# Kernel tuning notes

Measured on AMD Instinct MI355X. Metric: run time of the kernel, lower is better.

## Reference

```python
import jax, jax.numpy as jnp
import numpy as np

VOC, EMB, C, H, W, ANS = 10000, 300, 24, 8, 8, 1000
HID = 500          # lstm_hidden_size
GH = 100           # g_mlp hidden
B, L = 64, 32
O = H * W          # obj_num
CONCAT = 2 * C + HID  # 548


def setup_inputs() -> dict:
    key = jax.random.key(0)
    ks = jax.random.split(key, 20)
    inp = {}
    inp["sent_batch"] = jax.random.randint(ks[0], (B, L), 0, VOC)
    inp["conv_map_batch"] = jax.random.normal(ks[1], (B, C, H, W), jnp.float32)
    inp["sents_lengths"] = jax.random.randint(ks[2], (B,), 1, L + 1)
    # embedding table with padding_idx=0 zeroed
    emb = jax.random.normal(ks[3], (VOC, EMB), jnp.float32) * 0.02
    inp["embed_table"] = emb.at[0].set(0.0)
    # forward-direction LSTM params (torch gate order i,f,g,o)
    s_ih = 1.0 / np.sqrt(HID)
    inp["W_ih"] = jax.random.uniform(ks[4], (4 * HID, EMB), jnp.float32, -s_ih, s_ih)
    inp["W_hh"] = jax.random.uniform(ks[5], (4 * HID, HID), jnp.float32, -s_ih, s_ih)
    inp["b_ih"] = jax.random.uniform(ks[6], (4 * HID,), jnp.float32, -s_ih, s_ih)
    inp["b_hh"] = jax.random.uniform(ks[7], (4 * HID,), jnp.float32, -s_ih, s_ih)
    # random (non-learned) LSTM initial state, as torch.rand in init_hidden
    inp["h0"] = jax.random.uniform(ks[8], (B, HID), jnp.float32)
    inp["c0"] = jax.random.uniform(ks[9], (B, HID), jnp.float32)
    def lin(k, o, i):
        s = 1.0 / np.sqrt(i)
        kw, kb = jax.random.split(k)
        return (jax.random.uniform(kw, (o, i), jnp.float32, -s, s),
                jax.random.uniform(kb, (o,), jnp.float32, -s, s))
    inp["g1_w"], inp["g1_b"] = lin(ks[10], GH, CONCAT)
    inp["g2_w"], inp["g2_b"] = lin(ks[11], GH, GH)
    inp["f1_w"], inp["f1_b"] = lin(ks[12], GH, GH)
    inp["f2_w"], inp["f2_b"] = lin(ks[13], ANS, GH)
    return inp


def _lstm_final_h(emb, lengths, W_ih, W_hh, b_ih, b_hh, h0, c0):
    # emb: (B, L, EMB); returns final forward hidden at t = length-1 per example
    xs = jnp.swapaxes(emb, 0, 1)  # (L, B, EMB)
    ts = jnp.arange(emb.shape[1])
    bias = b_ih + b_hh
    def step(carry, inp):
        h, c = carry
        xt, t = inp
        gates = xt @ W_ih.T + h @ W_hh.T + bias
        i, f, g, o = jnp.split(gates, 4, axis=-1)
        i, f, o = jax.nn.sigmoid(i), jax.nn.sigmoid(f), jax.nn.sigmoid(o)
        g = jnp.tanh(g)
        c_new = f * c + i * g
        h_new = o * jnp.tanh(c_new)
        m = (t < lengths)[:, None]
        return (jnp.where(m, h_new, h), jnp.where(m, c_new, c)), None
    (h_T, _), _ = jax.lax.scan(step, (h0, c0), (xs, ts))
    return h_T  # (B, HID)


def reference(sent_batch, conv_map_batch, sents_lengths, embed_table,
              W_ih, W_hh, b_ih, b_hh, h0, c0,
              g1_w, g1_b, g2_w, g2_b, f1_w, f1_b, f2_w, f2_b):
    emb = embed_table[sent_batch]  # (B, L, EMB)
    q = _lstm_final_h(emb, sents_lengths, W_ih, W_hh, b_ih, b_hh, h0, c0)  # (B, HID)
    obj = jnp.transpose(conv_map_batch, (0, 2, 3, 1)).reshape(B, O, C)  # (B, O, C)
    # g_mlp layer 1, split to avoid materializing (B, O^2, 548):
    # pair (i,j): cat(q, obj_j, obj_i) -> partial sums broadcast-added
    q_part = q @ g1_w[:, :HID].T                    # (B, GH)
    j_part = obj @ g1_w[:, HID:HID + C].T           # (B, O, GH) -- conv_expand_1 block
    i_part = obj @ g1_w[:, HID + C:].T              # (B, O, GH) -- conv_expand_2 block
    h1 = jax.nn.relu(q_part[:, None, None, :] + i_part[:, :, None, :]
                     + j_part[:, None, :, :] + g1_b)  # (B, O, O, GH)
    h2 = jax.nn.relu(h1 @ g2_w.T + g2_b)              # (B, O, O, GH)
    g_sum = h2.sum(axis=(1, 2))                       # (B, GH)
    f = jax.nn.relu(g_sum @ f1_w.T + f1_b)
    f = jax.nn.relu(f @ f2_w.T + f2_b)                # (B, ANS)
    return jax.nn.log_softmax(f, axis=-1)
```

## Files before the change

kernel.cpp:

```cpp
#include <hip/hip_runtime.h>
#include <cmath>

#define BATCH 64
#define SEQL  32
#define EMBD  300
#define HIDD  500
#define NOBJ  64
#define GHID  100
#define ANSN  1000
#define MCOL  2048

#define GRP    4
#define GBATCH 16
#define BPG    25
#define UPB8   20
#define NBLK   (GRP*BPG)
#define SLOTP  32

#define KPADX  328
#define TCH    4

typedef _Float16 half8 __attribute__((ext_vector_type(8)));
typedef float    f32x4 __attribute__((ext_vector_type(4)));

__device__ __forceinline__ float sigmf(float x){ return 1.f/(1.f+expf(-x)); }

__device__ __forceinline__ unsigned long long ld_cc8(const unsigned long long* p){
    return __hip_atomic_load(p, __ATOMIC_RELAXED, __HIP_MEMORY_SCOPE_AGENT);
}
__device__ __forceinline__ void st_cc8(_Float16* p, unsigned long long v){
    __hip_atomic_store((unsigned long long*)p, v, __ATOMIC_RELAXED, __HIP_MEMORY_SCOPE_AGENT);
}

__global__ __launch_bounds__(256, 1) void k_xg2(
    const int* __restrict__ sent, const float* __restrict__ table,
    const float* __restrict__ Wih, const float* __restrict__ b_ih,
    const float* __restrict__ b_hh, float* __restrict__ xgT, int* __restrict__ slots)
{
    __shared__ _Float16 Sh[64*KPADX];
    __shared__ int sidx[TCH][64];
    int tid = threadIdx.x;
    int tc = blockIdx.x;
    int n0 = blockIdx.y * 64;
    int w = tid >> 6, lane = tid & 63;
    int rA = lane & 15, kb = lane >> 4;

    if (tc == 0 && blockIdx.y == 0 && tid < NBLK)
        __hip_atomic_store(slots + tid*SLOTP, 0, __ATOMIC_RELAXED, __HIP_MEMORY_SCOPE_AGENT);

    for (int i = tid; i < TCH*64; i += 256){
        int tt = i >> 6, b = i & 63;
        sidx[tt][b] = sent[b*SEQL + tc*TCH + tt];
    }
    for (int i = tid; i < 64*75; i += 256){
        int n = i / 75, c4 = i - (i/75)*75;
        float4 v = {0.f,0.f,0.f,0.f};
        if (n0 + n < 2000)
            v = *(const float4*)(Wih + (size_t)(n0+n)*300 + c4*4);
        _Float16* dst = &Sh[n*KPADX + c4*4];
        dst[0]=(_Float16)v.x; dst[1]=(_Float16)v.y; dst[2]=(_Float16)v.z; dst[3]=(_Float16)v.w;
    }
    for (int i = tid; i < 64*20; i += 256){
        int n = i / 20, k = 300 + (i - (i/20)*20);
        Sh[n*KPADX + k] = (_Float16)0.f;
    }
    __syncthreads();
    half8 areg[10];
    #pragma unroll
    for (int ks = 0; ks < 10; ++ks)
        areg[ks] = *(const half8*)&Sh[(w*16 + rA)*KPADX + ks*32 + kb*8];
    float biasr[4];
    #pragma unroll
    for (int r = 0; r < 4; ++r){
        int n = n0 + w*16 + kb*4 + r;
        biasr[r] = (n < 2000) ? b_ih[n] + b_hh[n] : 0.f;
    }
    __syncthreads();

    for (int tt = 0; tt < TCH; ++tt){
        for (int i = tid; i < 64*75; i += 256){
            int m = i / 75, c4 = i - (i/75)*75;
            float4 v = *(const float4*)(table + (size_t)sidx[tt][m]*300 + c4*4);
            _Float16* dst = &Sh[m*KPADX + c4*4];
            dst[0]=(_Float16)v.x; dst[1]=(_Float16)v.y; dst[2]=(_Float16)v.z; dst[3]=(_Float16)v.w;
        }
        for (int i = tid; i < 64*20; i += 256){
            int m = i / 20, k = 300 + (i - (i/20)*20);
            Sh[m*KPADX + k] = (_Float16)0.f;
        }
        __syncthreads();

        f32x4 acc[4] = {};
        #pragma unroll
        for (int ks = 0; ks < 10; ++ks){
            #pragma unroll
            for (int mc = 0; mc < 4; ++mc){
                half8 bf = *(const half8*)&Sh[(mc*16 + rA)*KPADX + ks*32 + kb*8];
                acc[mc] = __builtin_amdgcn_mfma_f32_16x16x32_f16(areg[ks], bf, acc[mc], 0, 0, 0);
            }
        }
        #pragma unroll
        for (int r = 0; r < 4; ++r){
            int n = n0 + w*16 + kb*4 + r;
            if (n < 2000){
                #pragma unroll
                for (int mc = 0; mc < 4; ++mc)
                    xgT[(size_t)n*MCOL + (tc*TCH+tt)*64 + mc*16 + rA] = acc[mc][r] + biasr[r];
            }
        }
        __syncthreads();
    }
}

__device__ __forceinline__ void gbarA(int* slots, int grp, int ub, int seq)
{
    __syncthreads();
    if (threadIdx.x == 0)
        __hip_atomic_store(slots + (grp*BPG + ub)*SLOTP, seq,
                           __ATOMIC_RELAXED, __HIP_MEMORY_SCOPE_AGENT);
    if (threadIdx.x < BPG){
        int* s = slots + (grp*BPG + threadIdx.x)*SLOTP;
        while (__hip_atomic_load(s, __ATOMIC_RELAXED, __HIP_MEMORY_SCOPE_AGENT) < seq)
            __builtin_amdgcn_s_sleep(1);
    }
    asm volatile("" ::: "memory");
    __syncthreads();
}

__global__ __launch_bounds__(320, 1) void k_lstm_v9(
    _Float16* __restrict__ hF, float* __restrict__ hqB,
    const float* __restrict__ xgT, const float* __restrict__ Whh,
    const float* __restrict__ h0, const float* __restrict__ c0,
    const int* __restrict__ lens, int* __restrict__ slots)
{
    __shared__ _Float16 Wl[80*512];
    __shared__ float    gl[4*80*16];
    __shared__ _Float16 hout[16*UPB8];

    int tid = threadIdx.x, bid = blockIdx.x;
    int grp = bid / BPG, ub = bid - grp*BPG;
    int u0  = ub * UPB8;
    int w   = tid >> 6, lane = tid & 63;

    int pb  = tid & 15, puu = tid >> 4;
    int pu  = u0 + puu;
    int gb  = grp*GBATCH + pb;
    float cprev = c0[gb*HIDD + pu];
    float hprev = h0[gb*HIDD + pu];
    int   mylen = lens[gb];
    hout[pb*UPB8 + puu] = (_Float16)hprev;

    for (int i = tid; i < 80*512; i += 320){
        int m = i >> 9, k = i & 511;
        int g = m / UPB8, uu = m - g*UPB8;
        float v = (k < HIDD) ? Whh[(size_t)(g*HIDD + u0 + uu)*HIDD + k] : 0.f;
        int off = (i*2) ^ ((m & 7) << 4);
        *(_Float16*)((char*)Wl + off) = (_Float16)v;
    }
    __syncthreads();
    if (tid < 80){
        int b = tid / 5, q = tid - (tid/5)*5;
        unsigned long long v = *(const unsigned long long*)((const char*)hout + b*40 + q*8);
        st_cc8(hF + ((size_t)(1*GRP + grp)*GBATCH + b)*512 + u0 + q*4, v);
    }
    if (ub == 0 && tid >= 128 && tid < 224){
        int j = tid - 128;
        int buf = j / 48, r = j - buf*48;
        int b = r / 3, q = r - (r/3)*3;
        st_cc8(hF + ((size_t)(buf*GRP + grp)*GBATCH + b)*512 + 500 + q*4, 0ULL);
    }
    gbarA(slots, grp, ub, 1);

    const int mA = lane & 15, kb = lane >> 4;

    for (int t = 0; t < SEQL; ++t){
        const _Float16* hsrc = hF + (size_t)(((t&1)^1)*GRP + grp)*GBATCH*512;

        float xgv[4];
        #pragma unroll
        for (int g = 0; g < 4; ++g)
            xgv[g] = xgT[(size_t)(g*HIDD + pu)*MCOL + t*64 + gb];

        if (w < 4){
            half8 bf[4];
            #pragma unroll
            for (int ks4 = 0; ks4 < 4; ++ks4){
                int ke = (w*4 + ks4)*32 + kb*8;
                const unsigned long long* p =
                    (const unsigned long long*)(hsrc + mA*512 + ke);
                union { unsigned long long q[2]; half8 h; } u;
                u.q[0] = ld_cc8(p);
                u.q[1] = ld_cc8(p + 1);
                bf[ks4] = u.h;
            }
            f32x4 acc[5] = {};
            #pragma unroll
            for (int rt = 0; rt < 5; ++rt){
                #pragma unroll
                for (int ks4 = 0; ks4 < 4; ++ks4){
                    int kByte = (w*4 + ks4)*64 + kb*16;
                    int m = rt*16 + mA;
                    int aOff = (m*1024 + kByte) ^ ((m & 7) << 4);
                    half8 af = *(const half8*)((const char*)Wl + aOff);
                    acc[rt] = __builtin_amdgcn_mfma_f32_16x16x32_f16(af, bf[ks4], acc[rt], 0, 0, 0);
                }
            }
            #pragma unroll
            for (int rt = 0; rt < 5; ++rt)
                #pragma unroll
                for (int r = 0; r < 4; ++r)
                    gl[(w*80 + rt*16 + kb*4 + r)*16 + mA] = acc[rt][r];
        }
        __syncthreads();

        {
            float g4[4];
            #pragma unroll
            for (int g = 0; g < 4; ++g){
                int row = g*UPB8 + puu;
                float s = gl[(0*80 + row)*16 + pb] + gl[(1*80 + row)*16 + pb]
                        + gl[(2*80 + row)*16 + pb] + gl[(3*80 + row)*16 + pb];
                s += xgv[g];
                g4[g] = s;
            }
            float si = sigmf(g4[0]), sf = sigmf(g4[1]);
            float tg = tanhf(g4[2]), so = sigmf(g4[3]);
            float cn = sf*cprev + si*tg;
            float hn = so*tanhf(cn);
            if (t < mylen){ cprev = cn; hprev = hn; }
            hout[pb*UPB8 + puu] = (_Float16)hprev;
            if (t == SEQL-1) hqB[(size_t)gb*512 + pu] = hprev;
        }
        if (t < SEQL-1){
            __syncthreads();
            if (tid < 80){
                int b = tid / 5, q = tid - (tid/5)*5;
                unsigned long long v = *(const unsigned long long*)((const char*)hout + b*40 + q*8);
                st_cc8(hF + ((size_t)((t&1)*GRP + grp)*GBATCH + b)*512 + u0 + q*4, v);
            }
            gbarA(slots, grp, ub, t + 2);
        }
    }
}

__global__ void k_qp(const float* __restrict__ hqB, const float* __restrict__ g1w,
                     const float* __restrict__ g1b, float* __restrict__ qp)
{
    int idx = blockIdx.x*blockDim.x + threadIdx.x;
    if (idx >= BATCH*GHID) return;
    int b = idx / GHID, n = idx % GHID;
    const float* wr = g1w + n*548;
    const float* hb = hqB + (size_t)b*512;
    float s = g1b[n];
    for (int k = 0; k < HIDD; ++k) s += hb[k]*wr[k];
    qp[idx] = s;
}

__global__ void k_ipjp(const float* __restrict__ conv, const float* __restrict__ g1w,
                       float* __restrict__ ip, float* __restrict__ jp)
{
    int idx = blockIdx.x*blockDim.x + threadIdx.x;
    if (idx >= BATCH*NOBJ*GHID) return;
    int b = idx / (NOBJ*GHID);
    int rem = idx - b*(NOBJ*GHID);
    int o = rem / GHID, n = rem % GHID;
    const float* wj = g1w + n*548 + 500;
    const float* wi = g1w + n*548 + 524;
    float si = 0.f, sj = 0.f;
    #pragma unroll
    for (int c = 0; c < 24; ++c){
        float v = conv[((size_t)b*24 + c)*NOBJ + o];
        sj += v*wj[c];
        si += v*wi[c];
    }
    ip[idx] = si;
    jp[idx] = sj;
}

__global__ __launch_bounds__(256, 1) void k_pair_mfma(
    const float* __restrict__ qp, const float* __restrict__ ip,
    const float* __restrict__ jp, const float* __restrict__ g2w,
    const float* __restrict__ g2b, float* __restrict__ part)
{
    __shared__ float    jpl[NOBJ][132];
    __shared__ float    basel[16][132];
    __shared__ _Float16 g2h[112][136];
    __shared__ float    redx[4][112];

    int b  = blockIdx.x >> 2;
    int ic = blockIdx.x & 3;
    int tid = threadIdx.x;
    int w = tid >> 6, lane = tid & 63;
    int ncol = lane & 15, kb = lane >> 4;

    for (int i = tid; i < NOBJ*100; i += 256){
        int j = i / 100, k = i - (i/100)*100;
        jpl[j][k] = jp[((size_t)b*NOBJ + j)*GHID + k];
    }
    for (int i = tid; i < NOBJ*32; i += 256)
        jpl[i >> 5][100 + (i & 31)] = 0.f;
    for (int i = tid; i < 16*100; i += 256){
        int il = i / 100, k = i - (i/100)*100;
        basel[il][k] = qp[b*GHID + k] + ip[((size_t)b*NOBJ + ic*16 + il)*GHID + k];
    }
    for (int i = tid; i < 16*32; i += 256)
        basel[i >> 5][100 + (i & 31)] = 0.f;
    for (int i = tid; i < 112*136; i += 256){
        int n = i / 136, k = i - (i/136)*136;
        g2h[n][k] = (n < 100 && k < 100) ? (_Float16)g2w[n*GHID + k] : (_Float16)0.f;
    }
    float gb7[7];
    #pragma unroll
    for (int nt = 0; nt < 7; ++nt){
        int n = nt*16 + ncol;
        gb7[nt] = (n < 100) ? g2b[n] : 0.f;
    }
    __syncthreads();

    f32x4 sacc[7] = {};
    #pragma unroll
    for (int it = 0; it < 4; ++it){
        int il = w*4 + it;
        #pragma unroll
        for (int jc = 0; jc < 4; ++jc){
            f32x4 acc[7] = {};
            int jrow = jc*16 + ncol;
            #pragma unroll
            for (int ks = 0; ks < 4; ++ks){
                int k0 = ks*32 + kb*8;
                const float* jpp = &jpl[jrow][k0];
                const float* bpp = &basel[il][k0];
                half8 af;
                #pragma unroll
                for (int e = 0; e < 8; ++e)
                    af[e] = (_Float16)fmaxf(jpp[e] + bpp[e], 0.f);
                #pragma unroll
                for (int nt = 0; nt < 7; ++nt){
                    half8 bf = *(const half8*)&g2h[nt*16 + ncol][k0];
                    acc[nt] = __builtin_amdgcn_mfma_f32_16x16x32_f16(af, bf, acc[nt], 0, 0, 0);
                }
            }
            #pragma unroll
            for (int nt = 0; nt < 7; ++nt)
                #pragma unroll
                for (int r = 0; r < 4; ++r)
                    sacc[nt][r] += fmaxf(acc[nt][r] + gb7[nt], 0.f);
        }
    }
    #pragma unroll
    for (int nt = 0; nt < 7; ++nt){
        float s = sacc[nt][0] + sacc[nt][1] + sacc[nt][2] + sacc[nt][3];
        s += __shfl_xor(s, 16);
        s += __shfl_xor(s, 32);
        if (lane < 16) redx[w][nt*16 + lane] = s;
    }
    __syncthreads();
    if (tid < 100){
        float p = redx[0][tid] + redx[1][tid] + redx[2][tid] + redx[3][tid];
        part[(size_t)(b*4 + ic)*GHID + tid] = p;
    }
}

__global__ __launch_bounds__(256) void k_final(const float* __restrict__ part, const float* __restrict__ f1w,
               const float* __restrict__ f1b, const float* __restrict__ f2w,
               const float* __restrict__ f2b, float* __restrict__ out)
{
    int b = blockIdx.x;
    int tid = threadIdx.x;
    __shared__ float gs[GHID];
    __shared__ float fh[GHID];
    __shared__ float lg[ANSN];
    __shared__ float red[4], red2[4];
    if (tid < GHID){
        float s = 0.f;
        for (int ic = 0; ic < 4; ++ic) s += part[((size_t)b*4 + ic)*GHID + tid];
        gs[tid] = s;
    }
    __syncthreads();
    if (tid < GHID){
        float s = f1b[tid];
        const float* w = f1w + tid*GHID;
        for (int k = 0; k < GHID; ++k) s += gs[k]*w[k];
        fh[tid] = fmaxf(s, 0.f);
    }
    __syncthreads();
    for (int n = tid; n < ANSN; n += 256){
        float s = f2b[n];
        const float* w = f2w + (size_t)n*GHID;
        for (int k = 0; k < GHID; ++k) s += fh[k]*w[k];
        lg[n] = fmaxf(s, 0.f);
    }
    __syncthreads();
    float mx = -1e30f;
    for (int n = tid; n < ANSN; n += 256) mx = fmaxf(mx, lg[n]);
    #pragma unroll
    for (int off = 32; off > 0; off >>= 1) mx = fmaxf(mx, __shfl_xor(mx, off));
    if ((tid & 63) == 0) red[tid >> 6] = mx;
    __syncthreads();
    mx = fmaxf(fmaxf(red[0], red[1]), fmaxf(red[2], red[3]));
    float se = 0.f;
    for (int n = tid; n < ANSN; n += 256) se += expf(lg[n]-mx);
    #pragma unroll
    for (int off = 32; off > 0; off >>= 1) se += __shfl_xor(se, off);
    if ((tid & 63) == 0) red2[tid >> 6] = se;
    __syncthreads();
    se = red2[0]+red2[1]+red2[2]+red2[3];
    float lse = logf(se);
    for (int n = tid; n < ANSN; n += 256) out[(size_t)b*ANSN + n] = lg[n] - mx - lse;
}

extern "C" void kernel_launch(void* const* d_in, const int* in_sizes, int n_in,
                              void* d_out, int out_size, void* d_ws, size_t ws_size,
                              hipStream_t stream)
{
    const int*   sent  = (const int*)  d_in[0];
    const float* conv  = (const float*)d_in[1];
    const int*   lens  = (const int*)  d_in[2];
    const float* table = (const float*)d_in[3];
    const float* W_ih  = (const float*)d_in[4];
    const float* W_hh  = (const float*)d_in[5];
    const float* b_ih  = (const float*)d_in[6];
    const float* b_hh  = (const float*)d_in[7];
    const float* h0    = (const float*)d_in[8];
    const float* c0    = (const float*)d_in[9];
    const float* g1_w  = (const float*)d_in[10];
    const float* g1_b  = (const float*)d_in[11];
    const float* g2_w  = (const float*)d_in[12];
    const float* g2_b  = (const float*)d_in[13];
    const float* f1_w  = (const float*)d_in[14];
    const float* f1_b  = (const float*)d_in[15];
    const float* f2_w  = (const float*)d_in[16];
    const float* f2_b  = (const float*)d_in[17];
    float* out = (float*)d_out;

    float* ws   = (float*)d_ws;
    int*   slots= (int*)d_ws;
    _Float16* hF = (_Float16*)(ws + 16384);
    float* hqB  = ws + 16384 + 32768;
    float* xgT  = hqB + 64*512;
    float* qp   = xgT + (size_t)4*HIDD*MCOL;
    float* ip   = qp  + BATCH*GHID;
    float* jp   = ip  + BATCH*NOBJ*GHID;
    float* part = jp  + BATCH*NOBJ*GHID;

    {
        dim3 g(SEQL/TCH, 32);
        k_xg2<<<g, 256, 0, stream>>>(sent, table, W_ih, b_ih, b_hh, xgT, slots);
    }

    k_lstm_v9<<<NBLK, 320, 0, stream>>>(hF, hqB, xgT, W_hh, h0, c0, lens, slots);

    k_qp<<<(BATCH*GHID + 255)/256, 256, 0, stream>>>(hqB, g1_w, g1_b, qp);
    k_ipjp<<<(BATCH*NOBJ*GHID + 255)/256, 256, 0, stream>>>(conv, g1_w, ip, jp);

    k_pair_mfma<<<BATCH*4, 256, 0, stream>>>(qp, ip, jp, g2_w, g2_b, part);

    k_final<<<BATCH, 256, 0, stream>>>(part, f1_w, f1_b, f2_w, f2_b, out);
}
```

Measured before the change: 262.4 us.

## Fuse q/i/j projection kernels into the pair MFMA kernel

Drops the separate k_qp and k_ipjp launches and computes the question projection and the per-object i/j projections inside the pair kernel from shared-memory copies of conv, g1 weights and the final hidden state. This removes two kernel launches and the global round trip of the ip/jp/qp intermediates. In exchange, each of the four blocks per batch recomputes the full jp table and qp, and an extra barrier is added before the main MFMA loop.

```diff
diff --git a/kernel.cpp b/kernel.cpp
--- a/kernel.cpp
+++ b/kernel.cpp
@@ -243,45 +243,16 @@
     }
 }
 
-__global__ void k_qp(const float* __restrict__ hqB, const float* __restrict__ g1w,
-                     const float* __restrict__ g1b, float* __restrict__ qp)
-{
-    int idx = blockIdx.x*blockDim.x + threadIdx.x;
-    if (idx >= BATCH*GHID) return;
-    int b = idx / GHID, n = idx % GHID;
-    const float* wr = g1w + n*548;
-    const float* hb = hqB + (size_t)b*512;
-    float s = g1b[n];
-    for (int k = 0; k < HIDD; ++k) s += hb[k]*wr[k];
-    qp[idx] = s;
-}
-
-__global__ void k_ipjp(const float* __restrict__ conv, const float* __restrict__ g1w,
-                       float* __restrict__ ip, float* __restrict__ jp)
-{
-    int idx = blockIdx.x*blockDim.x + threadIdx.x;
-    if (idx >= BATCH*NOBJ*GHID) return;
-    int b = idx / (NOBJ*GHID);
-    int rem = idx - b*(NOBJ*GHID);
-    int o = rem / GHID, n = rem % GHID;
-    const float* wj = g1w + n*548 + 500;
-    const float* wi = g1w + n*548 + 524;
-    float si = 0.f, sj = 0.f;
-    #pragma unroll
-    for (int c = 0; c < 24; ++c){
-        float v = conv[((size_t)b*24 + c)*NOBJ + o];
-        sj += v*wj[c];
-        si += v*wi[c];
-    }
-    ip[idx] = si;
-    jp[idx] = sj;
-}
-
-__global__ __launch_bounds__(256, 1) void k_pair_mfma(
-    const float* __restrict__ qp, const float* __restrict__ ip,
-    const float* __restrict__ jp, const float* __restrict__ g2w,
-    const float* __restrict__ g2b, float* __restrict__ part)
-{
+__global__ __launch_bounds__(256, 1) void k_pair2(
+    const float* __restrict__ hqB, const float* __restrict__ conv,
+    const float* __restrict__ g1w, const float* __restrict__ g1b,
+    const float* __restrict__ g2w, const float* __restrict__ g2b,
+    float* __restrict__ part)
+{
+    __shared__ float    convl[24][64];
+    __shared__ float    g1ij[100][48];
+    __shared__ float    hb[512];
+    __shared__ float    qpl[112];
     __shared__ float    jpl[NOBJ][132];
     __shared__ float    basel[16][132];
     __shared__ _Float16 g2h[112][136];
@@ -293,21 +264,50 @@
     int w = tid >> 6, lane = tid & 63;
     int ncol = lane & 15, kb = lane >> 4;
 
+    for (int i = tid; i < 24*64; i += 256)
+        convl[i>>6][i&63] = conv[((size_t)b*24 + (i>>6))*64 + (i&63)];
+    for (int i = tid; i < 100*48; i += 256){
+        int n = i/48, c = i - (i/48)*48;
+        g1ij[n][c] = g1w[(size_t)n*548 + 500 + c];
+    }
+    for (int i = tid; i < 512; i += 256) hb[i] = hqB[(size_t)b*512 + i];
+    for (int i = tid; i < 112*136; i += 256){
+        int n = i/136, k = i - (i/136)*136;
+        g2h[n][k] = (n < 100 && k < 100) ? (_Float16)g2w[n*GHID + k] : (_Float16)0.f;
+    }
+    __syncthreads();
+
+    if (tid < 100){
+        const float4* wr = (const float4*)(g1w + (size_t)tid*548);
+        float s = g1b[tid];
+        #pragma unroll 5
+        for (int k4 = 0; k4 < 125; ++k4){
+            float4 v = wr[k4];
+            s += v.x*hb[k4*4] + v.y*hb[k4*4+1] + v.z*hb[k4*4+2] + v.w*hb[k4*4+3];
+        }
+        qpl[tid] = s;
+    }
     for (int i = tid; i < NOBJ*100; i += 256){
-        int j = i / 100, k = i - (i/100)*100;
-        jpl[j][k] = jp[((size_t)b*NOBJ + j)*GHID + k];
-    }
-    for (int i = tid; i < NOBJ*32; i += 256)
-        jpl[i >> 5][100 + (i & 31)] = 0.f;
-    for (int i = tid; i < 16*100; i += 256){
-        int il = i / 100, k = i - (i/100)*100;
-        basel[il][k] = qp[b*GHID + k] + ip[((size_t)b*NOBJ + ic*16 + il)*GHID + k];
-    }
-    for (int i = tid; i < 16*32; i += 256)
-        basel[i >> 5][100 + (i & 31)] = 0.f;
-    for (int i = tid; i < 112*136; i += 256){
-        int n = i / 136, k = i - (i/136)*136;
-        g2h[n][k] = (n < 100 && k < 100) ? (_Float16)g2w[n*GHID + k] : (_Float16)0.f;
+        int o = i / 100, n = i - (i/100)*100;
+        float sj = 0.f;
+        #pragma unroll
+        for (int c = 0; c < 24; ++c) sj += convl[c][o] * g1ij[n][c];
+        jpl[o][n] = sj;
+    }
+    for (int i = tid; i < NOBJ*32; i += 256) jpl[i>>5][100 + (i&31)] = 0.f;
+    __syncthreads();
+
+    for (int i = tid; i < 16*132; i += 256){
+        int il = i / 132, k = i - (i/132)*132;
+        float v = 0.f;
+        if (k < 100){
+            float si = 0.f;
+            int o = ic*16 + il;
+            #pragma unroll
+            for (int c = 0; c < 24; ++c) si += convl[c][o] * g1ij[k][24+c];
+            v = qpl[k] + si;
+        }
+        basel[il][k] = v;
     }
     float gb7[7];
     #pragma unroll
@@ -438,10 +438,7 @@
     _Float16* hF = (_Float16*)(ws + 16384);
     float* hqB  = ws + 16384 + 32768;
     float* xgT  = hqB + 64*512;
-    float* qp   = xgT + (size_t)4*HIDD*MCOL;
-    float* ip   = qp  + BATCH*GHID;
-    float* jp   = ip  + BATCH*NOBJ*GHID;
-    float* part = jp  + BATCH*NOBJ*GHID;
+    float* part = xgT + (size_t)4*HIDD*MCOL;
 
     {
         dim3 g(SEQL/TCH, 32);
@@ -450,10 +447,7 @@
 
     k_lstm_v9<<<NBLK, 320, 0, stream>>>(hF, hqB, xgT, W_hh, h0, c0, lens, slots);
 
-    k_qp<<<(BATCH*GHID + 255)/256, 256, 0, stream>>>(hqB, g1_w, g1_b, qp);
-    k_ipjp<<<(BATCH*NOBJ*GHID + 255)/256, 256, 0, stream>>>(conv, g1_w, ip, jp);
-
-    k_pair_mfma<<<BATCH*4, 256, 0, stream>>>(qp, ip, jp, g2_w, g2_b, part);
+    k_pair2<<<BATCH*4, 256, 0, stream>>>(hqB, conv, g1_w, g1_b, g2_w, g2_b, part);
 
     k_final<<<BATCH, 256, 0, stream>>>(part, f1_w, f1_b, f2_w, f2_b, out);
 }
```

After: 258.3 us. About the same (-1.6%).
